# Optimization experiments

Measured on AMD Instinct MI355X. Metric: run time of the kernel, lower is better.

The kernel has to match this reference:

```python
import jax, jax.numpy as jnp
import numpy as np

L = 4  # num GIN layers
HID = 128
B_GRAPHS = 4096

def _bn(x, g, b, m, v):
    return (x - m) / jnp.sqrt(v + 1e-5) * g + b

def _ln(x, g, b):
    mu = jnp.mean(x, axis=-1, keepdims=True)
    var = jnp.var(x, axis=-1, keepdims=True)
    return (x - mu) / jnp.sqrt(var + 1e-5) * g + b

def _gin_encoder(x, ei, bat, aW, ab, eps, W1, b1, g1, be1, m1, v1, W2, b2, g2, be2, m2, v2):
    # x: [N,9], ei: [2,E], bat: [N]
    h = x @ aW + ab                                   # [N,HID]
    src, dst = ei[0], ei[1]
    for l in range(L):
        agg = jnp.zeros_like(h).at[dst].add(h[src])   # scatter-add neighbor sum
        z = (1.0 + eps[l]) * h + agg
        z = jax.nn.relu(_bn(z @ W1[l] + b1[l], g1[l], be1[l], m1[l], v1[l]))
        z = z @ W2[l] + b2[l]
        h = jax.nn.relu(_bn(z, g2[l], be2[l], m2[l], v2[l]))
    sums = jax.ops.segment_sum(h, bat, num_segments=B_GRAPHS)
    cnt = jax.ops.segment_sum(jnp.ones((h.shape[0],), h.dtype), bat, num_segments=B_GRAPHS)
    return sums / jnp.maximum(cnt, 1.0)[:, None]      # global_mean_pool -> [B,HID]

def reference(dx, de, db, sx, se, sb, t,
              enc_atom_W, enc_atom_b, enc_eps, enc_W1, enc_b1,
              enc_bn1_g, enc_bn1_b, enc_bn1_m, enc_bn1_v,
              enc_W2, enc_b2, enc_bn_g, enc_bn_b, enc_bn_m, enc_bn_v,
              temp_W1, temp_b1, temp_W2, temp_b2,
              int_W, int_b, int_ln_g, int_ln_b,
              fus_W1, fus_b1, fus_ln1_g, fus_ln1_b,
              fus_W2, fus_b2, fus_ln2_g, fus_ln2_b, fus_W3, fus_b3):
    # three encoders: [aq(drug), bs(drug), solvent], stacked on leading axis
    xs = jnp.stack([dx, dx, sx])      # [3,N,9]
    eis = jnp.stack([de, de, se])     # [3,2,E]
    bats = jnp.stack([db, db, sb])    # [3,N]
    embs = jax.vmap(_gin_encoder)(xs, eis, bats,
                                  enc_atom_W, enc_atom_b, enc_eps, enc_W1, enc_b1,
                                  enc_bn1_g, enc_bn1_b, enc_bn1_m, enc_bn1_v,
                                  enc_W2, enc_b2, enc_bn_g, enc_bn_b, enc_bn_m, enc_bn_v)
    aq, bs_, so = embs[0], embs[1], embs[2]           # each [B,HID]
    inter = jax.nn.relu(_ln(jnp.concatenate([bs_, so], axis=1) @ int_W + int_b, int_ln_g, int_ln_b))
    temp = jax.nn.relu(t @ temp_W1 + temp_b1) @ temp_W2 + temp_b2
    fusion = jnp.concatenate([aq, inter, temp], axis=1)  # [B, 2*HID+32]
    h = jax.nn.relu(_ln(fusion @ fus_W1 + fus_b1, fus_ln1_g, fus_ln1_b))
    h = jax.nn.relu(_ln(h @ fus_W2 + fus_b2, fus_ln2_g, fus_ln2_b))
    return h @ fus_W3 + fus_b3                        # [B,1]

def setup_inputs() -> dict:
    key = jax.random.key(0)
    ks = jax.random.split(key, 16)
    N, E, B = 50000, 600000, B_GRAPHS
    s = 0.1  # weight scale
    inp = {
        'dx': jax.random.normal(ks[0], (N, 9), jnp.float32),
        'de': jax.random.randint(ks[1], (2, E), 0, N),
        'db': jnp.sort(jax.random.randint(ks[2], (N,), 0, B)),
        'sx': jax.random.normal(ks[3], (N, 9), jnp.float32),
        'se': jax.random.randint(ks[4], (2, E), 0, N),
        'sb': jnp.sort(jax.random.randint(ks[5], (N,), 0, B)),
        't': jax.random.normal(ks[6], (B, 1), jnp.float32),
        'enc_atom_W': jax.random.normal(ks[7], (3, 9, HID), jnp.float32) * s,
        'enc_atom_b': jnp.zeros((3, HID), jnp.float32),
        'enc_eps': jnp.zeros((3, L), jnp.float32),
        'enc_W1': jax.random.normal(ks[8], (3, L, HID, 2 * HID), jnp.float32) * s,
        'enc_b1': jnp.zeros((3, L, 2 * HID), jnp.float32),
        'enc_bn1_g': jnp.ones((3, L, 2 * HID), jnp.float32),
        'enc_bn1_b': jnp.zeros((3, L, 2 * HID), jnp.float32),
        'enc_bn1_m': jnp.zeros((3, L, 2 * HID), jnp.float32),
        'enc_bn1_v': jnp.ones((3, L, 2 * HID), jnp.float32),
        'enc_W2': jax.random.normal(ks[9], (3, L, 2 * HID, HID), jnp.float32) * s,
        'enc_b2': jnp.zeros((3, L, HID), jnp.float32),
        'enc_bn_g': jnp.ones((3, L, HID), jnp.float32),
        'enc_bn_b': jnp.zeros((3, L, HID), jnp.float32),
        'enc_bn_m': jnp.zeros((3, L, HID), jnp.float32),
        'enc_bn_v': jnp.ones((3, L, HID), jnp.float32),
        'temp_W1': jax.random.normal(ks[10], (1, 32), jnp.float32) * s,
        'temp_b1': jnp.zeros((32,), jnp.float32),
        'temp_W2': jax.random.normal(ks[11], (32, 32), jnp.float32) * s,
        'temp_b2': jnp.zeros((32,), jnp.float32),
        'int_W': jax.random.normal(ks[12], (2 * HID, HID), jnp.float32) * s,
        'int_b': jnp.zeros((HID,), jnp.float32),
        'int_ln_g': jnp.ones((HID,), jnp.float32),
        'int_ln_b': jnp.zeros((HID,), jnp.float32),
        'fus_W1': jax.random.normal(ks[13], (2 * HID + 32, HID), jnp.float32) * s,
        'fus_b1': jnp.zeros((HID,), jnp.float32),
        'fus_ln1_g': jnp.ones((HID,), jnp.float32),
        'fus_ln1_b': jnp.zeros((HID,), jnp.float32),
        'fus_W2': jax.random.normal(ks[14], (HID, HID // 2), jnp.float32) * s,
        'fus_b2': jnp.zeros((HID // 2,), jnp.float32),
        'fus_ln2_g': jnp.ones((HID // 2,), jnp.float32),
        'fus_ln2_b': jnp.zeros((HID // 2,), jnp.float32),
        'fus_W3': jax.random.normal(ks[15], (HID // 2, 1), jnp.float32) * s,
        'fus_b3': jnp.zeros((1,), jnp.float32),
    }
    return inp
```

## Files before the change

### kernel.cpp

```cpp
#include <hip/hip_runtime.h>

#define HID 128
#define NLAYER 4

typedef unsigned short u16;
typedef __attribute__((ext_vector_type(8))) unsigned short u16x8;
typedef __attribute__((ext_vector_type(8))) short short8;
typedef __attribute__((ext_vector_type(4))) float floatx4;

__device__ __forceinline__ float bf2f(u16 u) {
    union { unsigned int i; float f; } v; v.i = ((unsigned int)u) << 16; return v.f;
}
__device__ __forceinline__ u16 f2bf(float f) {
    union { float f; unsigned int i; } v; v.f = f;
    unsigned int r = v.i + 0x7FFFu + ((v.i >> 16) & 1u);
    return (u16)(r >> 16);
}

__device__ __forceinline__ int lowbound(const int* __restrict__ a, int n, int v) {
    int lo = 0, hi = n;
    while (lo < hi) {
        int mid = (lo + hi) >> 1;
        if (a[mid] < v) lo = mid + 1; else hi = mid;
    }
    return lo;
}

__global__ void prep_weights(const float* __restrict__ W1, const float* __restrict__ W2,
                             u16* __restrict__ W1t, u16* __restrict__ W2t) {
    const int T = 3 * NLAYER * 128 * 256;
    int o = blockIdx.x * blockDim.x + threadIdx.x;
    if (o < T) {
        int k = o & 127, n = (o >> 7) & 255, el = o >> 15;
        W1t[o] = f2bf(W1[((size_t)el * 128 + k) * 256 + n]);
    } else if (o < 2 * T) {
        int o2 = o - T;
        int k = o2 & 255, n = (o2 >> 8) & 127, el = o2 >> 15;
        W2t[o2] = f2bf(W2[((size_t)el * 256 + k) * 128 + n]);
    }
}

__global__ void hist2(const int* __restrict__ de, const int* __restrict__ se,
                      int* __restrict__ cntd, int* __restrict__ cnts, int Ed, int Es) {
    const int g = blockIdx.y;
    const int* ei = g ? se : de;
    int* cnt = g ? cnts : cntd;
    const int E = g ? Es : Ed;
    int e = blockIdx.x * 256 + threadIdx.x;
    if (e < E) atomicAdd(&cnt[ei[E + e]], 1);
}

__global__ __launch_bounds__(256) void scan1v(const int* __restrict__ cntd,
                                              const int* __restrict__ cnts,
                                              int* __restrict__ bsumd,
                                              int* __restrict__ bsums, int N) {
    const int g = blockIdx.y;
    const int* cnt = g ? cnts : cntd;
    int* bsum = g ? bsums : bsumd;
    __shared__ int s[256];
    int i = blockIdx.x * 256 + threadIdx.x;
    s[threadIdx.x] = (i < N) ? cnt[i] : 0;
    __syncthreads();
    for (int o = 128; o > 0; o >>= 1) {
        if (threadIdx.x < o) s[threadIdx.x] += s[threadIdx.x + o];
        __syncthreads();
    }
    if (threadIdx.x == 0) bsum[blockIdx.x] = s[0];
}

__global__ __launch_bounds__(256) void scan2v(int* __restrict__ bsumd,
                                              int* __restrict__ bsums, int nb) {
    int* bsum = blockIdx.x ? bsums : bsumd;
    __shared__ int s[256];
    __shared__ int carry;
    if (threadIdx.x == 0) carry = 0;
    __syncthreads();
    for (int base = 0; base < nb; base += 256) {
        int i = base + threadIdx.x;
        int v = (i < nb) ? bsum[i] : 0;
        s[threadIdx.x] = v;
        __syncthreads();
        for (int o = 1; o < 256; o <<= 1) {
            int tv = (threadIdx.x >= o) ? s[threadIdx.x - o] : 0;
            __syncthreads();
            s[threadIdx.x] += tv;
            __syncthreads();
        }
        int excl = carry + s[threadIdx.x] - v;
        if (i < nb) bsum[i] = excl;
        __syncthreads();
        if (threadIdx.x == 0) carry += s[255];
        __syncthreads();
    }
}

__global__ __launch_bounds__(256) void scan3v(const int* __restrict__ cntd,
                                              const int* __restrict__ cnts,
                                              const int* __restrict__ bsumd,
                                              const int* __restrict__ bsums,
                                              int* __restrict__ rpd, int* __restrict__ rps,
                                              int N, int Ed, int Es) {
    const int g = blockIdx.y;
    const int* cnt = g ? cnts : cntd;
    const int* bsum = g ? bsums : bsumd;
    int* rowptr = g ? rps : rpd;
    const int E = g ? Es : Ed;
    __shared__ int s[256];
    int i = blockIdx.x * 256 + threadIdx.x;
    int v = (i < N) ? cnt[i] : 0;
    s[threadIdx.x] = v;
    __syncthreads();
    for (int o = 1; o < 256; o <<= 1) {
        int tv = (threadIdx.x >= o) ? s[threadIdx.x - o] : 0;
        __syncthreads();
        s[threadIdx.x] += tv;
        __syncthreads();
    }
    if (i < N) rowptr[i] = bsum[blockIdx.x] + s[threadIdx.x] - v;
    if (i == 0 && blockIdx.x == 0) rowptr[N] = E;
}

__global__ void fill2(const int* __restrict__ de, const int* __restrict__ se,
                      const int* __restrict__ rpd, const int* __restrict__ rps,
                      int* __restrict__ cnt2d, int* __restrict__ cnt2s,
                      int* __restrict__ sid, int* __restrict__ sis, int Ed, int Es) {
    const int g = blockIdx.y;
    const int* ei = g ? se : de;
    const int* rowptr = g ? rps : rpd;
    int* cnt2 = g ? cnt2s : cnt2d;
    int* srcidx = g ? sis : sid;
    const int E = g ? Es : Ed;
    int e = blockIdx.x * 256 + threadIdx.x;
    if (e < E) {
        const int dst = ei[E + e];
        const int pos = rowptr[dst] + atomicAdd(&cnt2[dst], 1);
        srcidx[pos] = ei[e];
    }
}

__global__ void atom_kernel(const float* __restrict__ dx, const float* __restrict__ sx,
                            const float* __restrict__ aW, const float* __restrict__ ab,
                            u16* __restrict__ h, int N) {
    const int slot = blockIdx.z;
    long idx = (long)blockIdx.x * blockDim.x + threadIdx.x;
    if (idx >= (long)N * HID) return;
    const int n = (int)(idx / HID), c = (int)(idx % HID);
    const float* x = (slot < 2) ? dx : sx;
    const float* W = aW + (size_t)slot * 9 * HID;
    float acc = ab[slot * HID + c];
#pragma unroll
    for (int k = 0; k < 9; k++) acc = fmaf(x[n * 9 + k], W[k * HID + c], acc);
    h[(size_t)slot * N * HID + idx] = f2bf(acc);
}

__global__ __launch_bounds__(256) void gather_agg(
    const int* __restrict__ rpd, const int* __restrict__ sid,
    const int* __restrict__ rps, const int* __restrict__ sis,
    const u16* __restrict__ h, u16* __restrict__ z,
    const float* __restrict__ eps, int N, int l) {
    const int slot = blockIdx.z;
    const int node = blockIdx.x * 16 + (threadIdx.x >> 4);
    if (node >= N) return;
    const int lane = threadIdx.x & 63;
    const int sl = lane & 15;
    const int subbase = lane & 48;
    const int* rowptr = (slot < 2) ? rpd : rps;
    const int* srcidx = (slot < 2) ? sid : sis;
    const int lo = rowptr[node], hi = rowptr[node + 1];
    const u16* hp = h + (size_t)slot * N * HID;
    const int coff = sl * 8;

    u16x8 hv = *(const u16x8*)(hp + (size_t)node * HID + coff);
    const float scale = 1.f + eps[slot * NLAYER + l];
    float s[8];
#pragma unroll
    for (int i = 0; i < 8; i++) s[i] = bf2f(hv[i]) * scale;

    for (int base = lo; base < hi; base += 16) {
        const int cnt = min(16, hi - base);
        int idx = (sl < cnt) ? srcidx[base + sl] : 0;
        int j = 0;
        for (; j + 4 <= cnt; j += 4) {
            const int s0 = __shfl(idx, subbase + j);
            const int s1 = __shfl(idx, subbase + j + 1);
            const int s2 = __shfl(idx, subbase + j + 2);
            const int s3 = __shfl(idx, subbase + j + 3);
            u16x8 v0 = *(const u16x8*)(hp + (size_t)s0 * HID + coff);
            u16x8 v1 = *(const u16x8*)(hp + (size_t)s1 * HID + coff);
            u16x8 v2 = *(const u16x8*)(hp + (size_t)s2 * HID + coff);
            u16x8 v3 = *(const u16x8*)(hp + (size_t)s3 * HID + coff);
#pragma unroll
            for (int i = 0; i < 8; i++)
                s[i] += (bf2f(v0[i]) + bf2f(v1[i])) + (bf2f(v2[i]) + bf2f(v3[i]));
        }
        for (; j < cnt; j++) {
            const int sj = __shfl(idx, subbase + j);
            u16x8 v = *(const u16x8*)(hp + (size_t)sj * HID + coff);
#pragma unroll
            for (int i = 0; i < 8; i++) s[i] += bf2f(v[i]);
        }
    }
    u16x8 o;
#pragma unroll
    for (int i = 0; i < 8; i++) o[i] = f2bf(s[i]);
    *(u16x8*)(z + (size_t)slot * N * HID + (size_t)node * HID + coff) = o;
}

__global__ __launch_bounds__(256, 2) void fused_layer(
    const u16* __restrict__ A, const u16* __restrict__ W1t, const u16* __restrict__ W2t,
    const float* __restrict__ b1, const float* __restrict__ g1, const float* __restrict__ be1,
    const float* __restrict__ m1, const float* __restrict__ v1,
    const float* __restrict__ b2, const float* __restrict__ g2, const float* __restrict__ be2,
    const float* __restrict__ m2, const float* __restrict__ v2,
    u16* __restrict__ out, int M, int l) {

    const int slot = blockIdx.z;
    const int m0 = blockIdx.x * 128;
    const u16* Ap  = A + (size_t)slot * M * 128;
    const int el = slot * NLAYER + l;
    const u16* Wp1 = W1t + (size_t)el * (256 * 128);
    const u16* Wp2 = W2t + (size_t)el * (128 * 256);
    const size_t poff1 = (size_t)el * 256;
    const size_t poff2 = (size_t)el * 128;

    __shared__ u16 sm[128 * 136];

    const int tid = threadIdx.x;
    const int lane = tid & 63;
    const int w = tid >> 6;
    const int sl = lane & 15;
    const int k8 = lane >> 4;

    {
        const int rp = tid >> 4;
        const int kc = (tid & 15) * 8;
#pragma unroll
        for (int p = 0; p < 8; p++) {
            const int row = p * 16 + rp;
            int gr = m0 + row; if (gr >= M) gr = M - 1;
            *(uint4*)&sm[row * 136 + kc] = *(const uint4*)(Ap + (size_t)gr * 128 + kc);
        }
    }
    __syncthreads();

    floatx4 acc1[8][4];
#pragma unroll
    for (int mt = 0; mt < 8; mt++)
#pragma unroll
        for (int c = 0; c < 4; c++) acc1[mt][c] = (floatx4)0.f;

#pragma unroll
    for (int ks = 0; ks < 4; ks++) {
        short8 a[8], b[4];
#pragma unroll
        for (int mt = 0; mt < 8; mt++)
            a[mt] = *(const short8*)&sm[(mt * 16 + sl) * 136 + ks * 32 + k8 * 8];
#pragma unroll
        for (int c = 0; c < 4; c++) {
            const int n = (c * 4 + w) * 16 + sl;
            b[c] = *(const short8*)(Wp1 + (size_t)n * 128 + ks * 32 + k8 * 8);
        }
#pragma unroll
        for (int mt = 0; mt < 8; mt++)
#pragma unroll
            for (int c = 0; c < 4; c++)
                acc1[mt][c] = __builtin_amdgcn_mfma_f32_16x16x32_bf16(a[mt], b[c], acc1[mt][c], 0, 0, 0);
    }
    __syncthreads();

    const int wr = w & 1, wc = w >> 1;
    floatx4 acc2[4][4];
#pragma unroll
    for (int mt = 0; mt < 4; mt++)
#pragma unroll
        for (int nt = 0; nt < 4; nt++) acc2[mt][nt] = (floatx4)0.f;

#pragma unroll
    for (int part = 0; part < 2; part++) {
#pragma unroll
        for (int c = part * 2; c < part * 2 + 2; c++) {
            const int gcol = (c * 4 + w) * 16 + sl;
            const int lcol = gcol - part * 128;
            const float sc = g1[poff1 + gcol] * rsqrtf(v1[poff1 + gcol] + 1e-5f);
            const float sh = (b1[poff1 + gcol] - m1[poff1 + gcol]) * sc + be1[poff1 + gcol];
#pragma unroll
            for (int mt = 0; mt < 8; mt++) {
#pragma unroll
                for (int r = 0; r < 4; r++) {
                    const int m = mt * 16 + k8 * 4 + r;
                    sm[m * 136 + lcol] = f2bf(fmaxf(fmaf(acc1[mt][c][r], sc, sh), 0.f));
                }
            }
        }
        __syncthreads();
#pragma unroll
        for (int ks = 0; ks < 4; ks++) {
            short8 a[4], b[4];
#pragma unroll
            for (int mt = 0; mt < 4; mt++)
                a[mt] = *(const short8*)&sm[(wr * 64 + mt * 16 + sl) * 136 + ks * 32 + k8 * 8];
#pragma unroll
            for (int nt = 0; nt < 4; nt++) {
                const int n = wc * 64 + nt * 16 + sl;
                b[nt] = *(const short8*)(Wp2 + (size_t)n * 256 + part * 128 + ks * 32 + k8 * 8);
            }
#pragma unroll
            for (int mt = 0; mt < 4; mt++)
#pragma unroll
                for (int nt = 0; nt < 4; nt++)
                    acc2[mt][nt] = __builtin_amdgcn_mfma_f32_16x16x32_bf16(a[mt], b[nt], acc2[mt][nt], 0, 0, 0);
        }
        if (part == 0) __syncthreads();
    }

    u16* outp = out + (size_t)slot * M * 128;
#pragma unroll
    for (int nt = 0; nt < 4; nt++) {
        const int col = wc * 64 + nt * 16 + sl;
        const float sc = g2[poff2 + col] * rsqrtf(v2[poff2 + col] + 1e-5f);
        const float sh = (b2[poff2 + col] - m2[poff2 + col]) * sc + be2[poff2 + col];
#pragma unroll
        for (int mt = 0; mt < 4; mt++) {
#pragma unroll
            for (int r = 0; r < 4; r++) {
                const int gr = m0 + wr * 64 + mt * 16 + k8 * 4 + r;
                if (gr < M)
                    outp[(size_t)gr * 128 + col] = f2bf(fmaxf(fmaf(acc2[mt][nt][r], sc, sh), 0.f));
            }
        }
    }
}

__global__ __launch_bounds__(128) void pool_kernel(const int* __restrict__ db,
                                                   const int* __restrict__ sb,
                                                   const u16* __restrict__ h,
                                                   float* __restrict__ emb,
                                                   int N, int B) {
    const int slot = blockIdx.z;
    const int* bat = (slot < 2) ? db : sb;
    const int g = blockIdx.x;
    const int lo = lowbound(bat, N, g);
    const int hi = lowbound(bat, N, g + 1);
    const int c = threadIdx.x;
    float s = 0.f;
    const u16* hp = h + (size_t)slot * N * HID;
    for (int n = lo; n < hi; n++) s += bf2f(hp[(size_t)n * HID + c]);
    const float cnt = (float)(hi - lo);
    emb[((size_t)slot * B + g) * HID + c] = s / fmaxf(cnt, 1.f);
}

__device__ __forceinline__ float block_sum128(float x, float* red, int tid) {
    red[tid] = x;
    __syncthreads();
    if (tid < 64) {
        float v = red[tid] + red[tid + 64];
#pragma unroll
        for (int o = 32; o > 0; o >>= 1) v += __shfl_down(v, o);
        if (tid == 0) red[0] = v;
    }
    __syncthreads();
    float r = red[0];
    __syncthreads();
    return r;
}

__global__ __launch_bounds__(128) void fusion_kernel(
    const float* __restrict__ emb, const float* __restrict__ t,
    const float* __restrict__ tW1, const float* __restrict__ tb1,
    const float* __restrict__ tW2, const float* __restrict__ tb2,
    const float* __restrict__ iW, const float* __restrict__ ib,
    const float* __restrict__ ilg, const float* __restrict__ ilb,
    const float* __restrict__ fW1, const float* __restrict__ fb1,
    const float* __restrict__ l1g, const float* __restrict__ l1b,
    const float* __restrict__ fW2, const float* __restrict__ fb2,
    const float* __restrict__ l2g, const float* __restrict__ l2b,
    const float* __restrict__ fW3, const float* __restrict__ fb3,
    float* __restrict__ out, int B) {
    const int r = blockIdx.x;
    const int tid = threadIdx.x;
    __shared__ float cs[256];
    __shared__ float cat[288];
    __shared__ float buf[128];
    __shared__ float red[128];
    __shared__ float tmp32[32];

    cs[tid]        = emb[((size_t)1 * B + r) * HID + tid];
    cs[128 + tid]  = emb[((size_t)2 * B + r) * HID + tid];
    cat[tid]       = emb[((size_t)0 * B + r) * HID + tid];
    __syncthreads();

    float acc = ib[tid];
    for (int k = 0; k < 256; k++) acc = fmaf(cs[k], iW[k * HID + tid], acc);
    float mu  = block_sum128(acc, red, tid) * (1.f / 128.f);
    float d   = acc - mu;
    float var = block_sum128(d * d, red, tid) * (1.f / 128.f);
    float inter = fmaxf(d * rsqrtf(var + 1e-5f) * ilg[tid] + ilb[tid], 0.f);
    cat[128 + tid] = inter;

    if (tid < 32) tmp32[tid] = fmaxf(fmaf(t[r], tW1[tid], tb1[tid]), 0.f);
    __syncthreads();
    if (tid < 32) {
        float a2 = tb2[tid];
        for (int j = 0; j < 32; j++) a2 = fmaf(tmp32[j], tW2[j * 32 + tid], a2);
        cat[256 + tid] = a2;
    }
    __syncthreads();

    float a1 = fb1[tid];
    for (int k = 0; k < 288; k++) a1 = fmaf(cat[k], fW1[k * HID + tid], a1);
    mu  = block_sum128(a1, red, tid) * (1.f / 128.f);
    d   = a1 - mu;
    var = block_sum128(d * d, red, tid) * (1.f / 128.f);
    buf[tid] = fmaxf(d * rsqrtf(var + 1e-5f) * l1g[tid] + l1b[tid], 0.f);
    __syncthreads();

    float a2v = 0.f;
    if (tid < 64) {
        a2v = fb2[tid];
        for (int k = 0; k < 128; k++) a2v = fmaf(buf[k], fW2[k * 64 + tid], a2v);
    }
    mu = block_sum128((tid < 64) ? a2v : 0.f, red, tid) * (1.f / 64.f);
    float d2 = (tid < 64) ? (a2v - mu) : 0.f;
    var = block_sum128(d2 * d2, red, tid) * (1.f / 64.f);
    float contrib = 0.f;
    if (tid < 64) {
        float h2 = fmaxf(d2 * rsqrtf(var + 1e-5f) * l2g[tid] + l2b[tid], 0.f);
        contrib = h2 * fW3[tid];
    }
    float s = block_sum128(contrib, red, tid);
    if (tid == 0) out[r] = s + fb3[0];
}

extern "C" void kernel_launch(void* const* d_in, const int* in_sizes, int n_in,
                              void* d_out, int out_size, void* d_ws, size_t ws_size,
                              hipStream_t stream) {
    const float* dx  = (const float*)d_in[0];
    const int*   de  = (const int*)d_in[1];
    const int*   db  = (const int*)d_in[2];
    const float* sx  = (const float*)d_in[3];
    const int*   se  = (const int*)d_in[4];
    const int*   sb  = (const int*)d_in[5];
    const float* t   = (const float*)d_in[6];
    const float* aW  = (const float*)d_in[7];
    const float* ab  = (const float*)d_in[8];
    const float* eps = (const float*)d_in[9];
    const float* W1  = (const float*)d_in[10];
    const float* b1  = (const float*)d_in[11];
    const float* g1  = (const float*)d_in[12];
    const float* be1 = (const float*)d_in[13];
    const float* m1  = (const float*)d_in[14];
    const float* v1  = (const float*)d_in[15];
    const float* W2  = (const float*)d_in[16];
    const float* b2  = (const float*)d_in[17];
    const float* g2  = (const float*)d_in[18];
    const float* be2 = (const float*)d_in[19];
    const float* m2  = (const float*)d_in[20];
    const float* v2  = (const float*)d_in[21];
    const float* tW1 = (const float*)d_in[22];
    const float* tb1 = (const float*)d_in[23];
    const float* tW2 = (const float*)d_in[24];
    const float* tb2 = (const float*)d_in[25];
    const float* iW  = (const float*)d_in[26];
    const float* ib  = (const float*)d_in[27];
    const float* ilg = (const float*)d_in[28];
    const float* ilb = (const float*)d_in[29];
    const float* fW1 = (const float*)d_in[30];
    const float* fb1 = (const float*)d_in[31];
    const float* l1g = (const float*)d_in[32];
    const float* l1b = (const float*)d_in[33];
    const float* fW2 = (const float*)d_in[34];
    const float* fb2 = (const float*)d_in[35];
    const float* l2g = (const float*)d_in[36];
    const float* l2b = (const float*)d_in[37];
    const float* fW3 = (const float*)d_in[38];
    const float* fb3 = (const float*)d_in[39];
    float* out = (float*)d_out;

    const int N  = in_sizes[0] / 9;
    const int Ed = in_sizes[1] / 2;
    const int Es = in_sizes[4] / 2;
    const int B  = in_sizes[6];
    const int nb = (N + 255) / 256;
    const int Emax = (Ed > Es) ? Ed : Es;

    char* w8 = (char*)d_ws;
    int* rpd   = (int*)w8;
    int* rps   = rpd + (N + 1);
    int* cntd  = rps + (N + 1);
    int* cnts  = cntd + N;
    int* cnt2d = cnts + N;
    int* cnt2s = cnt2d + N;
    int* sid   = cnt2s + N;
    int* sis   = sid + Ed;
    int* bsumd = sis + Es;
    int* bsums = bsumd + nb;
    size_t int_bytes = ((char*)(bsums + nb)) - w8;
    size_t foff = (int_bytes + 255) & ~(size_t)255;

    const int WT = 3 * NLAYER * 128 * 256;
    u16* W1t = (u16*)(w8 + foff);
    u16* W2t = W1t + WT;
    const size_t hS = (size_t)N * HID;
    u16* hbuf = W2t + WT;
    u16* zbuf = hbuf + 3 * hS;
    float* emb = (float*)(((uintptr_t)(zbuf + 3 * hS) + 255) & ~(uintptr_t)255);

    prep_weights<<<(2 * WT + 255) / 256, 256, 0, stream>>>(W1, W2, W1t, W2t);
    hipMemsetAsync(cntd, 0, (size_t)4 * N * sizeof(int), stream);
    {
        dim3 gh((Emax + 255) / 256, 2);
        hist2<<<gh, 256, 0, stream>>>(de, se, cntd, cnts, Ed, Es);
        dim3 gs1(nb, 2);
        scan1v<<<gs1, 256, 0, stream>>>(cntd, cnts, bsumd, bsums, N);
        scan2v<<<2, 256, 0, stream>>>(bsumd, bsums, nb);
        scan3v<<<gs1, 256, 0, stream>>>(cntd, cnts, bsumd, bsums, rpd, rps, N, Ed, Es);
        fill2<<<gh, 256, 0, stream>>>(de, se, rpd, rps, cnt2d, cnt2s, sid, sis, Ed, Es);
    }

    {
        dim3 ga((N * HID + 255) / 256, 1, 3);
        atom_kernel<<<ga, 256, 0, stream>>>(dx, sx, aW, ab, hbuf, N);
        for (int l = 0; l < NLAYER; l++) {
            dim3 gg((N + 15) / 16, 1, 3);
            gather_agg<<<gg, 256, 0, stream>>>(rpd, sid, rps, sis, hbuf, zbuf, eps, N, l);
            dim3 gf((N + 127) / 128, 1, 3);
            fused_layer<<<gf, 256, 0, stream>>>(zbuf, W1t, W2t,
                                                b1, g1, be1, m1, v1,
                                                b2, g2, be2, m2, v2,
                                                hbuf, N, l);
        }
        dim3 gp(B, 1, 3);
        pool_kernel<<<gp, 128, 0, stream>>>(db, sb, hbuf, emb, N, B);
    }
    fusion_kernel<<<B, 128, 0, stream>>>(emb, t, tW1, tb1, tW2, tb2,
                                         iW, ib, ilg, ilb, fW1, fb1, l1g, l1b,
                                         fW2, fb2, l2g, l2b, fW3, fb3, out, B);
}
```

Before: 839.6 us.

## Fuse neighbor aggregation into GIN MLP layer kernel and simplify CSR fill

The separate gather_agg kernel is removed. The neighbor-sum aggregation now runs inside the fused MLP kernel, which writes the aggregated rows straight into shared memory before the MFMA GEMMs, and h is ping-ponged between two buffers. This drops the round trip of the aggregated z tensor through global memory and one launch per layer. In exchange, the gather runs at the GEMM kernel's lower occupancy (launch_bounds 256,2), which may hide gather latency less well. Separately, the CSR fill now uses a cursor array initialized by the scan, replacing the rowptr read plus a count atomic, and the memset shrinks.

New measurement: 995.9 us. 1.19x slower.

```diff
diff --git a/kernel.cpp b/kernel.cpp
--- a/kernel.cpp
+++ b/kernel.cpp
@@ -99,11 +99,13 @@
                                               const int* __restrict__ bsumd,
                                               const int* __restrict__ bsums,
                                               int* __restrict__ rpd, int* __restrict__ rps,
+                                              int* __restrict__ curd, int* __restrict__ curs,
                                               int N, int Ed, int Es) {
     const int g = blockIdx.y;
     const int* cnt = g ? cnts : cntd;
     const int* bsum = g ? bsums : bsumd;
     int* rowptr = g ? rps : rpd;
+    int* cur = g ? curs : curd;
     const int E = g ? Es : Ed;
     __shared__ int s[256];
     int i = blockIdx.x * 256 + threadIdx.x;
@@ -116,24 +118,26 @@
         s[threadIdx.x] += tv;
         __syncthreads();
     }
-    if (i < N) rowptr[i] = bsum[blockIdx.x] + s[threadIdx.x] - v;
+    if (i < N) {
+        const int st = bsum[blockIdx.x] + s[threadIdx.x] - v;
+        rowptr[i] = st;
+        cur[i] = st;
+    }
     if (i == 0 && blockIdx.x == 0) rowptr[N] = E;
 }
 
 __global__ void fill2(const int* __restrict__ de, const int* __restrict__ se,
-                      const int* __restrict__ rpd, const int* __restrict__ rps,
-                      int* __restrict__ cnt2d, int* __restrict__ cnt2s,
+                      int* __restrict__ curd, int* __restrict__ curs,
                       int* __restrict__ sid, int* __restrict__ sis, int Ed, int Es) {
     const int g = blockIdx.y;
     const int* ei = g ? se : de;
-    const int* rowptr = g ? rps : rpd;
-    int* cnt2 = g ? cnt2s : cnt2d;
+    int* cur = g ? curs : curd;
     int* srcidx = g ? sis : sid;
     const int E = g ? Es : Ed;
     int e = blockIdx.x * 256 + threadIdx.x;
     if (e < E) {
         const int dst = ei[E + e];
-        const int pos = rowptr[dst] + atomicAdd(&cnt2[dst], 1);
+        const int pos = atomicAdd(&cur[dst], 1);
         srcidx[pos] = ei[e];
     }
 }
@@ -153,61 +157,11 @@
     h[(size_t)slot * N * HID + idx] = f2bf(acc);
 }
 
-__global__ __launch_bounds__(256) void gather_agg(
+__global__ __launch_bounds__(256, 2) void fused_gin_layer(
     const int* __restrict__ rpd, const int* __restrict__ sid,
     const int* __restrict__ rps, const int* __restrict__ sis,
-    const u16* __restrict__ h, u16* __restrict__ z,
-    const float* __restrict__ eps, int N, int l) {
-    const int slot = blockIdx.z;
-    const int node = blockIdx.x * 16 + (threadIdx.x >> 4);
-    if (node >= N) return;
-    const int lane = threadIdx.x & 63;
-    const int sl = lane & 15;
-    const int subbase = lane & 48;
-    const int* rowptr = (slot < 2) ? rpd : rps;
-    const int* srcidx = (slot < 2) ? sid : sis;
-    const int lo = rowptr[node], hi = rowptr[node + 1];
-    const u16* hp = h + (size_t)slot * N * HID;
-    const int coff = sl * 8;
-
-    u16x8 hv = *(const u16x8*)(hp + (size_t)node * HID + coff);
-    const float scale = 1.f + eps[slot * NLAYER + l];
-    float s[8];
-#pragma unroll
-    for (int i = 0; i < 8; i++) s[i] = bf2f(hv[i]) * scale;
-
-    for (int base = lo; base < hi; base += 16) {
-        const int cnt = min(16, hi - base);
-        int idx = (sl < cnt) ? srcidx[base + sl] : 0;
-        int j = 0;
-        for (; j + 4 <= cnt; j += 4) {
-            const int s0 = __shfl(idx, subbase + j);
-            const int s1 = __shfl(idx, subbase + j + 1);
-            const int s2 = __shfl(idx, subbase + j + 2);
-            const int s3 = __shfl(idx, subbase + j + 3);
-            u16x8 v0 = *(const u16x8*)(hp + (size_t)s0 * HID + coff);
-            u16x8 v1 = *(const u16x8*)(hp + (size_t)s1 * HID + coff);
-            u16x8 v2 = *(const u16x8*)(hp + (size_t)s2 * HID + coff);
-            u16x8 v3 = *(const u16x8*)(hp + (size_t)s3 * HID + coff);
-#pragma unroll
-            for (int i = 0; i < 8; i++)
-                s[i] += (bf2f(v0[i]) + bf2f(v1[i])) + (bf2f(v2[i]) + bf2f(v3[i]));
-        }
-        for (; j < cnt; j++) {
-            const int sj = __shfl(idx, subbase + j);
-            u16x8 v = *(const u16x8*)(hp + (size_t)sj * HID + coff);
-#pragma unroll
-            for (int i = 0; i < 8; i++) s[i] += bf2f(v[i]);
-        }
-    }
-    u16x8 o;
-#pragma unroll
-    for (int i = 0; i < 8; i++) o[i] = f2bf(s[i]);
-    *(u16x8*)(z + (size_t)slot * N * HID + (size_t)node * HID + coff) = o;
-}
-
-__global__ __launch_bounds__(256, 2) void fused_layer(
     const u16* __restrict__ A, const u16* __restrict__ W1t, const u16* __restrict__ W2t,
+    const float* __restrict__ eps,
     const float* __restrict__ b1, const float* __restrict__ g1, const float* __restrict__ be1,
     const float* __restrict__ m1, const float* __restrict__ v1,
     const float* __restrict__ b2, const float* __restrict__ g2, const float* __restrict__ be2,
@@ -216,6 +170,8 @@
 
     const int slot = blockIdx.z;
     const int m0 = blockIdx.x * 128;
+    const int* rowptr = (slot < 2) ? rpd : rps;
+    const int* srcidx = (slot < 2) ? sid : sis;
     const u16* Ap  = A + (size_t)slot * M * 128;
     const int el = slot * NLAYER + l;
     const u16* Wp1 = W1t + (size_t)el * (256 * 128);
@@ -233,12 +189,50 @@
 
     {
         const int rp = tid >> 4;
-        const int kc = (tid & 15) * 8;
-#pragma unroll
+        const int subbase = lane & 48;
+        const int coff = sl * 8;
+        const float scale = 1.f + eps[slot * NLAYER + l];
         for (int p = 0; p < 8; p++) {
             const int row = p * 16 + rp;
-            int gr = m0 + row; if (gr >= M) gr = M - 1;
-            *(uint4*)&sm[row * 136 + kc] = *(const uint4*)(Ap + (size_t)gr * 128 + kc);
+            const int gr = m0 + row;
+            float s[8];
+            if (gr < M) {
+                u16x8 hv = *(const u16x8*)(Ap + (size_t)gr * 128 + coff);
+#pragma unroll
+                for (int i = 0; i < 8; i++) s[i] = bf2f(hv[i]) * scale;
+                const int lo = rowptr[gr], hi = rowptr[gr + 1];
+                for (int base = lo; base < hi; base += 16) {
+                    const int cnt = min(16, hi - base);
+                    int idx = (sl < cnt) ? srcidx[base + sl] : 0;
+                    int j = 0;
+                    for (; j + 4 <= cnt; j += 4) {
+                        const int s0 = __shfl(idx, subbase + j);
+                        const int s1 = __shfl(idx, subbase + j + 1);
+                        const int s2 = __shfl(idx, subbase + j + 2);
+                        const int s3 = __shfl(idx, subbase + j + 3);
+                        u16x8 v0 = *(const u16x8*)(Ap + (size_t)s0 * 128 + coff);
+                        u16x8 v1 = *(const u16x8*)(Ap + (size_t)s1 * 128 + coff);
+                        u16x8 v2 = *(const u16x8*)(Ap + (size_t)s2 * 128 + coff);
+                        u16x8 v3 = *(const u16x8*)(Ap + (size_t)s3 * 128 + coff);
+#pragma unroll
+                        for (int i = 0; i < 8; i++)
+                            s[i] += (bf2f(v0[i]) + bf2f(v1[i])) + (bf2f(v2[i]) + bf2f(v3[i]));
+                    }
+                    for (; j < cnt; j++) {
+                        const int sj = __shfl(idx, subbase + j);
+                        u16x8 v = *(const u16x8*)(Ap + (size_t)sj * 128 + coff);
+#pragma unroll
+                        for (int i = 0; i < 8; i++) s[i] += bf2f(v[i]);
+                    }
+                }
+            } else {
+#pragma unroll
+                for (int i = 0; i < 8; i++) s[i] = 0.f;
+            }
+            u16x8 o;
+#pragma unroll
+            for (int i = 0; i < 8; i++) o[i] = f2bf(s[i]);
+            *(u16x8*)&sm[row * 136 + coff] = o;
         }
     }
     __syncthreads();
@@ -488,9 +482,9 @@
     int* rps   = rpd + (N + 1);
     int* cntd  = rps + (N + 1);
     int* cnts  = cntd + N;
-    int* cnt2d = cnts + N;
-    int* cnt2s = cnt2d + N;
-    int* sid   = cnt2s + N;
+    int* curd  = cnts + N;
+    int* curs  = curd + N;
+    int* sid   = curs + N;
     int* sis   = sid + Ed;
     int* bsumd = sis + Es;
     int* bsums = bsumd + nb;
@@ -506,31 +500,32 @@
     float* emb = (float*)(((uintptr_t)(zbuf + 3 * hS) + 255) & ~(uintptr_t)255);
 
     prep_weights<<<(2 * WT + 255) / 256, 256, 0, stream>>>(W1, W2, W1t, W2t);
-    hipMemsetAsync(cntd, 0, (size_t)4 * N * sizeof(int), stream);
+    hipMemsetAsync(cntd, 0, (size_t)2 * N * sizeof(int), stream);
     {
         dim3 gh((Emax + 255) / 256, 2);
         hist2<<<gh, 256, 0, stream>>>(de, se, cntd, cnts, Ed, Es);
         dim3 gs1(nb, 2);
         scan1v<<<gs1, 256, 0, stream>>>(cntd, cnts, bsumd, bsums, N);
         scan2v<<<2, 256, 0, stream>>>(bsumd, bsums, nb);
-        scan3v<<<gs1, 256, 0, stream>>>(cntd, cnts, bsumd, bsums, rpd, rps, N, Ed, Es);
-        fill2<<<gh, 256, 0, stream>>>(de, se, rpd, rps, cnt2d, cnt2s, sid, sis, Ed, Es);
+        scan3v<<<gs1, 256, 0, stream>>>(cntd, cnts, bsumd, bsums, rpd, rps, curd, curs, N, Ed, Es);
+        fill2<<<gh, 256, 0, stream>>>(de, se, curd, curs, sid, sis, Ed, Es);
     }
 
     {
         dim3 ga((N * HID + 255) / 256, 1, 3);
         atom_kernel<<<ga, 256, 0, stream>>>(dx, sx, aW, ab, hbuf, N);
+        u16* cur = hbuf;
+        u16* nxt = zbuf;
         for (int l = 0; l < NLAYER; l++) {
-            dim3 gg((N + 15) / 16, 1, 3);
-            gather_agg<<<gg, 256, 0, stream>>>(rpd, sid, rps, sis, hbuf, zbuf, eps, N, l);
             dim3 gf((N + 127) / 128, 1, 3);
-            fused_layer<<<gf, 256, 0, stream>>>(zbuf, W1t, W2t,
-                                                b1, g1, be1, m1, v1,
-                                                b2, g2, be2, m2, v2,
-                                                hbuf, N, l);
+            fused_gin_layer<<<gf, 256, 0, stream>>>(rpd, sid, rps, sis, cur, W1t, W2t, eps,
+                                                    b1, g1, be1, m1, v1,
+                                                    b2, g2, be2, m2, v2,
+                                                    nxt, N, l);
+            u16* tsw = cur; cur = nxt; nxt = tsw;
         }
         dim3 gp(B, 1, 3);
-        pool_kernel<<<gp, 128, 0, stream>>>(db, sb, hbuf, emb, N, B);
+        pool_kernel<<<gp, 128, 0, stream>>>(db, sb, cur, emb, N, B);
     }
     fusion_kernel<<<B, 128, 0, stream>>>(emb, t, tW1, tb1, tW2, tb2,
                                          iW, ib, ilg, ilb, fW1, fb1, l1g, l1b,
```
